# Performance work log

Hardware: AMD Instinct MI355X
Metric: run time of the kernel (lower is better)

The kernel has to match this reference:

```python
import jax, jax.numpy as jnp
import numpy as np

NEG_BIG = -1e12
ALPHA = 0.2  # LeakyReLU negative slope

def setup_inputs() -> dict:
    key = jax.random.key(0)
    k1, k2, k3, k4, k5 = jax.random.split(key, 5)
    N, F_in, F_out = 8192, 256, 128
    inp = jax.random.normal(k1, (N, F_in), dtype=jnp.float32)
    adj = jax.random.randint(k2, (N, N), 0, 2, dtype=jnp.int32)
    W = jax.random.normal(k3, (F_in, F_out), dtype=jnp.float32) * 0.05
    W_2 = jax.random.normal(k4, (F_in, F_out), dtype=jnp.float32) * 0.05
    W_3 = jax.random.normal(k5, (F_in, F_out), dtype=jnp.float32) * 0.05
    return {"inp": inp, "adj": adj, "W": W, "W_2": W_2, "W_3": W_3}

def reference(inp, adj, W, W_2, W_3):
    # h = inp @ W, h_2 = inp @ W_2  -> scores e = LeakyReLU(h @ h_2^T)  [N, N]
    h = inp @ W
    h_2 = inp @ W_2
    e = jax.nn.leaky_relu(h @ h_2.T, negative_slope=ALPHA)
    # adjacency mask, row softmax (dropout disabled: eval mode)
    attention = jax.nn.softmax(jnp.where(adj > 0, e, NEG_BIG), axis=1)
    h_3 = inp @ W_3
    h_prime = attention @ h_3
    return jax.nn.elu(h_prime)  # concat=True path
```

## Files before the change

kernel.cpp:

```cpp
#include <hip/hip_runtime.h>
#include <hip/hip_fp16.h>

#define N    8192
#define FIN  256
#define FOUT 128
#define BN   64

typedef _Float16 half8 __attribute__((ext_vector_type(8)));
typedef _Float16 half4v __attribute__((ext_vector_type(4)));
typedef float floatx4 __attribute__((ext_vector_type(4)));

__global__ __launch_bounds__(256)
void maskprep_kernel(const int* __restrict__ adj,
                     unsigned long long* __restrict__ Msk2)
{
    const int wave = threadIdx.x >> 6;
    const int lane = threadIdx.x & 63;
    const int row  = blockIdx.x * 4 + wave;
    const int* base = adj + (size_t)row * N;
    for (int g = 0; g < 128; g++) {
        int v = base[g * 64 + lane];
        unsigned long long b = __ballot(v != 0);
        if (lane == 0) Msk2[(size_t)g * N + row] = b;
    }
}

__global__ __launch_bounds__(256)
void wprep_kernel(const float* __restrict__ W0,
                  const float* __restrict__ W1,
                  const float* __restrict__ W2,
                  _Float16* __restrict__ Wf)
{
    int idx  = blockIdx.x * 256 + threadIdx.x;
    int lane = idx & 63;
    int frag = idx >> 6;
    int w    = frag >> 6;
    int f    = frag & 63;
    int nt   = f >> 3, kc = f & 7;
    int quad = lane >> 4, lo16 = lane & 15;
    const float* Wp = w == 0 ? W0 : (w == 1 ? W1 : W2);
    half8 v;
#pragma unroll
    for (int jj = 0; jj < 8; jj++)
        v[jj] = (_Float16)Wp[(size_t)(kc * 32 + quad * 8 + jj) * FOUT + nt * 16 + lo16];
    *(half8*)&Wf[(size_t)idx * 8] = v;
}

__global__ __launch_bounds__(256, 2)
void gemm3_kernel(const float* __restrict__ inp,
                  const _Float16* __restrict__ Wf,
                  _Float16* __restrict__ H,
                  _Float16* __restrict__ H2,
                  _Float16* __restrict__ H3T)
{
    const int which = blockIdx.z;
    const int c0    = blockIdx.y * 64;
    const _Float16* Wfw = Wf + (size_t)which * 64 * 64 * 8;
    const int r0 = blockIdx.x * 64;
    const int tid  = threadIdx.x;
    const int wave = tid >> 6;
    const int lane = tid & 63;
    const int lo16 = lane & 15;
    const int quad = lane >> 4;
    const int r = r0 + wave * 16 + lo16;

    half8 a[8];
#pragma unroll
    for (int kc = 0; kc < 8; kc++) {
        const float* p = &inp[(size_t)r * FIN + kc * 32 + quad * 8];
        float4 v0 = *(const float4*)p;
        float4 v1 = *(const float4*)(p + 4);
        a[kc][0] = (_Float16)v0.x; a[kc][1] = (_Float16)v0.y;
        a[kc][2] = (_Float16)v0.z; a[kc][3] = (_Float16)v0.w;
        a[kc][4] = (_Float16)v1.x; a[kc][5] = (_Float16)v1.y;
        a[kc][6] = (_Float16)v1.z; a[kc][7] = (_Float16)v1.w;
    }

    floatx4 acc[4];
#pragma unroll
    for (int i = 0; i < 4; i++) acc[i] = (floatx4){0.f, 0.f, 0.f, 0.f};

#pragma unroll
    for (int kc = 0; kc < 8; kc++)
#pragma unroll
        for (int nt = 0; nt < 4; nt++) {
            int ntg = (c0 >> 4) + nt;
            half8 b = *(const half8*)&Wfw[(((size_t)ntg * 8 + kc) * 64 + lane) * 8];
            acc[nt] = __builtin_amdgcn_mfma_f32_16x16x32_f16(a[kc], b, acc[nt], 0, 0, 0);
        }

    const int arow = wave * 16 + quad * 4;
    if (which < 2) {
        _Float16* outp = which == 0 ? H : H2;
#pragma unroll
        for (int nt = 0; nt < 4; nt++)
#pragma unroll
            for (int rr = 0; rr < 4; rr++)
                outp[(size_t)(r0 + arow + rr) * FOUT + c0 + nt * 16 + lo16] = (_Float16)acc[nt][rr];
    } else {
#pragma unroll
        for (int nt = 0; nt < 4; nt++) {
            half4v v;
#pragma unroll
            for (int rr = 0; rr < 4; rr++) v[rr] = (_Float16)acc[nt][rr];
            *(half4v*)&H3T[(size_t)(c0 + nt * 16 + lo16) * N + r0 + arow] = v;
        }
    }
}

__global__ __launch_bounds__(256)
void repackK_kernel(const _Float16* __restrict__ H2, _Float16* __restrict__ Kf)
{
    int idx  = blockIdx.x * 256 + threadIdx.x;
    int lane = idx & 63;
    int frag = idx >> 6;
    int jb = frag >> 4, f = frag & 15;
    int c = f >> 3, ntj = (f >> 2) & 1, kc = f & 3;
    int quad = lane >> 4, lo16 = lane & 15;
    int srcrow = jb * 64 + c * 32 + (lo16 >> 2) * 8 + ntj * 4 + (lo16 & 3);
    half8 v = *(const half8*)&H2[(size_t)srcrow * FOUT + kc * 32 + quad * 8];
    *(half8*)&Kf[(size_t)idx * 8] = v;
}

__global__ __launch_bounds__(256)
void repackV_kernel(const _Float16* __restrict__ H3T, _Float16* __restrict__ Vf)
{
    int idx  = blockIdx.x * 256 + threadIdx.x;
    int lane = idx & 63;
    int frag = idx >> 6;
    int jb = frag >> 4, f = frag & 15, nt = f >> 1, kc = f & 1;
    int quad = lane >> 4, lo16 = lane & 15;
    half8 v = *(const half8*)&H3T[(size_t)(nt * 16 + lo16) * N + jb * 64 + kc * 32 + quad * 8];
    *(half8*)&Vf[(size_t)idx * 8] = v;
}

template<int JS>
__global__ __launch_bounds__(256, 2)
void attn_kernel(const _Float16* __restrict__ Hq,
                 const _Float16* __restrict__ Kf,
                 const _Float16* __restrict__ Vf,
                 const unsigned long long* __restrict__ Msk2,
                 float* __restrict__ OpartT,
                 float* __restrict__ mpart,
                 float* __restrict__ lpart)
{
    __shared__ _Float16 KV[2][16384];

    const int tid  = threadIdx.x;
    const int wave = tid >> 6;
    const int lane = tid & 63;
    const int lo16 = lane & 15;
    const int quad = lane >> 4;
    const int bid  = blockIdx.x;
    const int js   = bid & (JS - 1);
    const int ib   = bid / JS;
    const int i0   = ib * 128;
    const int iw   = i0 + wave * 32;
    const int jbeg = js * (N / JS);
    const int NIT  = (N / JS) / BN;

    half8 q[2][4];
#pragma unroll
    for (int isub = 0; isub < 2; isub++)
#pragma unroll
        for (int kc = 0; kc < 4; kc++)
            q[isub][kc] = *(const half8*)&Hq[(size_t)(iw + isub * 16 + lo16) * FOUT + kc * 32 + quad * 8];

    floatx4 O[8][2];
#pragma unroll
    for (int nt = 0; nt < 8; nt++)
#pragma unroll
        for (int s = 0; s < 2; s++) O[nt][s] = (floatx4){0.f, 0.f, 0.f, 0.f};
    float m_s[2] = {-1e12f, -1e12f}, l_s[2] = {0.f, 0.f};

    {
        const int jb0 = jbeg >> 6;
        const _Float16* gk = Kf + (size_t)jb0 * 8192;
        const _Float16* gv = Vf + (size_t)jb0 * 8192;
#pragma unroll
        for (int r = 0; r < 4; r++) {
            int off = (r * 256 + tid) * 8;
            *(half8*)&KV[0][off]        = *(const half8*)&gk[off];
            *(half8*)&KV[0][8192 + off] = *(const half8*)&gv[off];
        }
        __syncthreads();
    }

    int cur = 0;
    for (int it = 0; it < NIT; it++) {
        const int j0 = jbeg + it * BN;

        half8 st[8];
        if (it + 1 < NIT) {
            const int jbn = (j0 + BN) >> 6;
            const _Float16* gk = Kf + (size_t)jbn * 8192;
            const _Float16* gv = Vf + (size_t)jbn * 8192;
#pragma unroll
            for (int r = 0; r < 4; r++) {
                int off = (r * 256 + tid) * 8;
                st[r]     = *(const half8*)&gk[off];
                st[r + 4] = *(const half8*)&gv[off];
            }
        }
        unsigned long long mw[2];
        mw[0] = Msk2[(size_t)(j0 >> 6) * N + iw + lo16];
        mw[1] = Msk2[(size_t)(j0 >> 6) * N + iw + 16 + lo16];

        const _Float16* kb = &KV[cur][0];
        const _Float16* vb = &KV[cur][8192];

        floatx4 S[2][2][2];
#pragma unroll
        for (int c = 0; c < 2; c++)
#pragma unroll
            for (int ntj = 0; ntj < 2; ntj++) {
                S[c][ntj][0] = (floatx4){0.f, 0.f, 0.f, 0.f};
                S[c][ntj][1] = (floatx4){0.f, 0.f, 0.f, 0.f};
#pragma unroll
                for (int kc = 0; kc < 4; kc++) {
                    half8 kf = *(const half8*)&kb[(((c * 2 + ntj) * 4 + kc) * 64 + lane) * 8];
                    S[c][ntj][0] = __builtin_amdgcn_mfma_f32_16x16x32_f16(kf, q[0][kc], S[c][ntj][0], 0, 0, 0);
                    S[c][ntj][1] = __builtin_amdgcn_mfma_f32_16x16x32_f16(kf, q[1][kc], S[c][ntj][1], 0, 0, 0);
                }
            }

        float ev[2][2][2][4];
#pragma unroll
        for (int c = 0; c < 2; c++)
#pragma unroll
            for (int ntj = 0; ntj < 2; ntj++)
#pragma unroll
                for (int s = 0; s < 2; s++)
#pragma unroll
                    for (int r = 0; r < 4; r++) {
                        float e = S[c][ntj][s][r];
                        ev[c][ntj][s][r] = e > 0.f ? e : 0.2f * e;
                    }

        float alpha[2];
#pragma unroll
        for (int s = 0; s < 2; s++) {
            float mx = ev[0][0][s][0];
#pragma unroll
            for (int c = 0; c < 2; c++)
#pragma unroll
                for (int ntj = 0; ntj < 2; ntj++)
#pragma unroll
                    for (int r = 0; r < 4; r++)
                        mx = fmaxf(mx, ev[c][ntj][s][r]);
            mx = fmaxf(mx, __shfl_xor(mx, 16));
            mx = fmaxf(mx, __shfl_xor(mx, 32));
            float mn = fmaxf(m_s[s], mx);
            alpha[s] = __expf(m_s[s] - mn);
            m_s[s] = mn;
        }

        half8 pb[2][2];
        float sum[2] = {0.f, 0.f};
#pragma unroll
        for (int s = 0; s < 2; s++) {
            unsigned long long mq = mw[s] >> (quad * 8);
#pragma unroll
            for (int c = 0; c < 2; c++)
#pragma unroll
                for (int ntj = 0; ntj < 2; ntj++)
#pragma unroll
                    for (int r = 0; r < 4; r++) {
                        bool bit = (mq >> (c * 32 + ntj * 4 + r)) & 1ull;
                        float p = bit ? __expf(ev[c][ntj][s][r] - m_s[s]) : 0.f;
                        sum[s] += p;
                        pb[s][c][ntj * 4 + r] = (_Float16)p;
                    }
            sum[s] += __shfl_xor(sum[s], 16);
            sum[s] += __shfl_xor(sum[s], 32);
            l_s[s] = l_s[s] * alpha[s] + sum[s];
#pragma unroll
            for (int nt = 0; nt < 8; nt++)
#pragma unroll
                for (int r = 0; r < 4; r++)
                    O[nt][s][r] *= alpha[s];
        }

#pragma unroll
        for (int c = 0; c < 2; c++)
#pragma unroll
            for (int nt = 0; nt < 8; nt++) {
                half8 vf = *(const half8*)&vb[((nt * 2 + c) * 64 + lane) * 8];
                O[nt][0] = __builtin_amdgcn_mfma_f32_16x16x32_f16(vf, pb[0][c], O[nt][0], 0, 0, 0);
                O[nt][1] = __builtin_amdgcn_mfma_f32_16x16x32_f16(vf, pb[1][c], O[nt][1], 0, 0, 0);
            }

        if (it + 1 < NIT) {
            const int nxt = cur ^ 1;
#pragma unroll
            for (int r = 0; r < 4; r++) {
                int off = (r * 256 + tid) * 8;
                *(half8*)&KV[nxt][off]        = st[r];
                *(half8*)&KV[nxt][8192 + off] = st[r + 4];
            }
        }
        __syncthreads();
        cur ^= 1;
    }

#pragma unroll
    for (int nt = 0; nt < 8; nt++)
#pragma unroll
        for (int s = 0; s < 2; s++)
#pragma unroll
            for (int r = 0; r < 4; r++) {
                int f = nt * 16 + quad * 4 + r;
                int i = iw + s * 16 + lo16;
                OpartT[((size_t)js * FOUT + f) * N + i] = O[nt][s][r];
            }
    if (quad == 0) {
#pragma unroll
        for (int s = 0; s < 2; s++) {
            mpart[js * N + iw + s * 16 + lo16] = m_s[s];
            lpart[js * N + iw + s * 16 + lo16] = l_s[s];
        }
    }
}

template<int JS>
__global__ __launch_bounds__(256)
void combine_kernel(const float* __restrict__ OpartT,
                    const float* __restrict__ mpart,
                    const float* __restrict__ lpart,
                    float* __restrict__ out)
{
    int idx = blockIdx.x * 256 + threadIdx.x;
    int f  = idx >> 11;
    int i4 = (idx & 2047) << 2;

    float4 M = {-3e38f, -3e38f, -3e38f, -3e38f};
    float4 m[JS];
#pragma unroll
    for (int s = 0; s < JS; s++) {
        m[s] = *(const float4*)&mpart[s * N + i4];
        M.x = fmaxf(M.x, m[s].x); M.y = fmaxf(M.y, m[s].y);
        M.z = fmaxf(M.z, m[s].z); M.w = fmaxf(M.w, m[s].w);
    }
    float4 L = {0.f, 0.f, 0.f, 0.f};
    float4 w[JS];
#pragma unroll
    for (int s = 0; s < JS; s++) {
        float4 l = *(const float4*)&lpart[s * N + i4];
        w[s].x = __expf(m[s].x - M.x); w[s].y = __expf(m[s].y - M.y);
        w[s].z = __expf(m[s].z - M.z); w[s].w = __expf(m[s].w - M.w);
        L.x += l.x * w[s].x; L.y += l.y * w[s].y;
        L.z += l.z * w[s].z; L.w += l.w * w[s].w;
    }
    float4 o = {0.f, 0.f, 0.f, 0.f};
#pragma unroll
    for (int s = 0; s < JS; s++) {
        float4 v = *(const float4*)&OpartT[((size_t)s * FOUT + f) * N + i4];
        o.x += w[s].x * v.x; o.y += w[s].y * v.y;
        o.z += w[s].z * v.z; o.w += w[s].w * v.w;
    }
    float r0 = o.x / L.x, r1 = o.y / L.y, r2 = o.z / L.z, r3 = o.w / L.w;
    out[(size_t)(i4 + 0) * FOUT + f] = r0 > 0.f ? r0 : __expf(r0) - 1.f;
    out[(size_t)(i4 + 1) * FOUT + f] = r1 > 0.f ? r1 : __expf(r1) - 1.f;
    out[(size_t)(i4 + 2) * FOUT + f] = r2 > 0.f ? r2 : __expf(r2) - 1.f;
    out[(size_t)(i4 + 3) * FOUT + f] = r3 > 0.f ? r3 : __expf(r3) - 1.f;
}

extern "C" void kernel_launch(void* const* d_in, const int* in_sizes, int n_in,
                              void* d_out, int out_size, void* d_ws, size_t ws_size,
                              hipStream_t stream) {
    const float* inp = (const float*)d_in[0];
    const int*   adj = (const int*)d_in[1];
    const float* W0  = (const float*)d_in[2];
    const float* W1  = (const float*)d_in[3];
    const float* W2  = (const float*)d_in[4];
    float* out = (float*)d_out;

    constexpr int JS = 8;
    char* ws = (char*)d_ws;
    _Float16* H    = (_Float16*)(ws);
    _Float16* H2   = (_Float16*)(ws + (2u << 20));
    _Float16* H3T  = (_Float16*)(ws + (4u << 20));
    _Float16* Wf   = (_Float16*)(ws + (6u << 20));
    unsigned long long* Msk2 = (unsigned long long*)(ws + (7u << 20));
    _Float16* Kf   = (_Float16*)(ws + (15u << 20));
    _Float16* Vf   = (_Float16*)(ws + (17u << 20));
    float* OpartT  = (float*)(ws + (19u << 20));
    float* mpart   = (float*)(ws + (51u << 20));
    float* lpart   = (float*)(ws + (51u << 20) + (size_t)JS * N * sizeof(float));

    maskprep_kernel<<<N / 4, 256, 0, stream>>>(adj, Msk2);
    wprep_kernel<<<48, 256, 0, stream>>>(W0, W1, W2, Wf);
    gemm3_kernel<<<dim3(N / 64, 2, 3), 256, 0, stream>>>(inp, Wf, H, H2, H3T);
    repackK_kernel<<<512, 256, 0, stream>>>(H2, Kf);
    repackV_kernel<<<512, 256, 0, stream>>>(H3T, Vf);
    attn_kernel<JS><<<(N / 128) * JS, 256, 0, stream>>>(H, Kf, Vf, Msk2, OpartT, mpart, lpart);
    combine_kernel<JS><<<(FOUT * (N / 4)) / 256, 256, 0, stream>>>(OpartT, mpart, lpart, out);
}
```

Before: 486.7 us.

## Fuse adjacency bitmask construction into attention kernel, drop maskprep pass

Removes the separate maskprep kernel, which read the 256MB int32 adjacency and wrote a packed bitmask. The attention kernel now loads the raw adjacency ints for its 32 rows x 64 columns per iteration and builds the per-lane masks with ballots. LeakyReLU is recomputed instead of stored, to save registers. This removes one kernel launch and the bitmask write and read-back, but the adjacency loads (32 ints per lane) now sit inside the attention loop and add register pressure and latency there.

```diff
diff --git a/kernel.cpp b/kernel.cpp
--- a/kernel.cpp
+++ b/kernel.cpp
@@ -9,21 +9,6 @@
 typedef _Float16 half8 __attribute__((ext_vector_type(8)));
 typedef _Float16 half4v __attribute__((ext_vector_type(4)));
 typedef float floatx4 __attribute__((ext_vector_type(4)));
-
-__global__ __launch_bounds__(256)
-void maskprep_kernel(const int* __restrict__ adj,
-                     unsigned long long* __restrict__ Msk2)
-{
-    const int wave = threadIdx.x >> 6;
-    const int lane = threadIdx.x & 63;
-    const int row  = blockIdx.x * 4 + wave;
-    const int* base = adj + (size_t)row * N;
-    for (int g = 0; g < 128; g++) {
-        int v = base[g * 64 + lane];
-        unsigned long long b = __ballot(v != 0);
-        if (lane == 0) Msk2[(size_t)g * N + row] = b;
-    }
-}
 
 __global__ __launch_bounds__(256)
 void wprep_kernel(const float* __restrict__ W0,
@@ -139,7 +124,7 @@
 void attn_kernel(const _Float16* __restrict__ Hq,
                  const _Float16* __restrict__ Kf,
                  const _Float16* __restrict__ Vf,
-                 const unsigned long long* __restrict__ Msk2,
+                 const int* __restrict__ adj,
                  float* __restrict__ OpartT,
                  float* __restrict__ mpart,
                  float* __restrict__ lpart)
@@ -190,6 +175,13 @@
     for (int it = 0; it < NIT; it++) {
         const int j0 = jbeg + it * BN;
 
+        int av[32];
+        {
+            const int* ap = adj + (size_t)iw * N + j0 + lane;
+#pragma unroll
+            for (int x = 0; x < 32; x++) av[x] = ap[(size_t)x * N];
+        }
+
         half8 st[8];
         if (it + 1 < NIT) {
             const int jbn = (j0 + BN) >> 6;
@@ -202,9 +194,6 @@
                 st[r + 4] = *(const half8*)&gv[off];
             }
         }
-        unsigned long long mw[2];
-        mw[0] = Msk2[(size_t)(j0 >> 6) * N + iw + lo16];
-        mw[1] = Msk2[(size_t)(j0 >> 6) * N + iw + 16 + lo16];
 
         const _Float16* kb = &KV[cur][0];
         const _Float16* vb = &KV[cur][8192];
@@ -224,30 +213,20 @@
                 }
             }
 
-        float ev[2][2][2][4];
-#pragma unroll
-        for (int c = 0; c < 2; c++)
-#pragma unroll
-            for (int ntj = 0; ntj < 2; ntj++)
-#pragma unroll
-                for (int s = 0; s < 2; s++)
+        float alpha[2];
+#pragma unroll
+        for (int s = 0; s < 2; s++) {
+            float mx = -1e12f;
+#pragma unroll
+            for (int c = 0; c < 2; c++)
+#pragma unroll
+                for (int ntj = 0; ntj < 2; ntj++)
 #pragma unroll
                     for (int r = 0; r < 4; r++) {
                         float e = S[c][ntj][s][r];
-                        ev[c][ntj][s][r] = e > 0.f ? e : 0.2f * e;
+                        e = e > 0.f ? e : 0.2f * e;
+                        mx = fmaxf(mx, e);
                     }
-
-        float alpha[2];
-#pragma unroll
-        for (int s = 0; s < 2; s++) {
-            float mx = ev[0][0][s][0];
-#pragma unroll
-            for (int c = 0; c < 2; c++)
-#pragma unroll
-                for (int ntj = 0; ntj < 2; ntj++)
-#pragma unroll
-                    for (int r = 0; r < 4; r++)
-                        mx = fmaxf(mx, ev[c][ntj][s][r]);
             mx = fmaxf(mx, __shfl_xor(mx, 16));
             mx = fmaxf(mx, __shfl_xor(mx, 32));
             float mn = fmaxf(m_s[s], mx);
@@ -255,6 +234,17 @@
             m_s[s] = mn;
         }
 
+        unsigned long long mw0 = 0, mw1 = 0;
+#pragma unroll
+        for (int x = 0; x < 16; x++) {
+            unsigned long long b0 = __ballot(av[x] != 0);
+            unsigned long long b1 = __ballot(av[x + 16] != 0);
+            bool sel = (lo16 == x);
+            mw0 = sel ? b0 : mw0;
+            mw1 = sel ? b1 : mw1;
+        }
+        unsigned long long mw[2] = {mw0, mw1};
+
         half8 pb[2][2];
         float sum[2] = {0.f, 0.f};
 #pragma unroll
@@ -266,8 +256,10 @@
                 for (int ntj = 0; ntj < 2; ntj++)
 #pragma unroll
                     for (int r = 0; r < 4; r++) {
+                        float e = S[c][ntj][s][r];
+                        e = e > 0.f ? e : 0.2f * e;
                         bool bit = (mq >> (c * 32 + ntj * 4 + r)) & 1ull;
-                        float p = bit ? __expf(ev[c][ntj][s][r] - m_s[s]) : 0.f;
+                        float p = bit ? __expf(e - m_s[s]) : 0.f;
                         sum[s] += p;
                         pb[s][c][ntj * 4 + r] = (_Float16)p;
                     }
@@ -381,18 +373,16 @@
     _Float16* H2   = (_Float16*)(ws + (2u << 20));
     _Float16* H3T  = (_Float16*)(ws + (4u << 20));
     _Float16* Wf   = (_Float16*)(ws + (6u << 20));
-    unsigned long long* Msk2 = (unsigned long long*)(ws + (7u << 20));
-    _Float16* Kf   = (_Float16*)(ws + (15u << 20));
-    _Float16* Vf   = (_Float16*)(ws + (17u << 20));
-    float* OpartT  = (float*)(ws + (19u << 20));
-    float* mpart   = (float*)(ws + (51u << 20));
-    float* lpart   = (float*)(ws + (51u << 20) + (size_t)JS * N * sizeof(float));
-
-    maskprep_kernel<<<N / 4, 256, 0, stream>>>(adj, Msk2);
+    _Float16* Kf   = (_Float16*)(ws + (7u << 20));
+    _Float16* Vf   = (_Float16*)(ws + (9u << 20));
+    float* OpartT  = (float*)(ws + (11u << 20));
+    float* mpart   = (float*)(ws + (43u << 20));
+    float* lpart   = (float*)(ws + (43u << 20) + (size_t)JS * N * sizeof(float));
+
     wprep_kernel<<<48, 256, 0, stream>>>(W0, W1, W2, Wf);
     gemm3_kernel<<<dim3(N / 64, 2, 3), 256, 0, stream>>>(inp, Wf, H, H2, H3T);
     repackK_kernel<<<512, 256, 0, stream>>>(H2, Kf);
     repackV_kernel<<<512, 256, 0, stream>>>(H3T, Vf);
-    attn_kernel<JS><<<(N / 128) * JS, 256, 0, stream>>>(H, Kf, Vf, Msk2, OpartT, mpart, lpart);
+    attn_kernel<JS><<<(N / 128) * JS, 256, 0, stream>>>(H, Kf, Vf, adj, OpartT, mpart, lpart);
     combine_kernel<JS><<<(FOUT * (N / 4)) / 256, 256, 0, stream>>>(OpartT, mpart, lpart, out);
 }
```

Measured after the change: 432.6 us. 1.12x faster.
